# Kernel tuning notes

Hardware: AMD Instinct MI355X
Metric: run time of the kernel (lower is better)

## Reference

```python
import jax, jax.numpy as jnp
import numpy as np

N_NODES = 100000
N_EDGES = 1600000
D_IN = 64
D_OUT = 64


def setup_inputs() -> dict:
    key = jax.random.key(0)
    k1, k2, k3 = jax.random.split(key, 3)
    edge_index = jax.random.randint(k1, (2, N_EDGES), 0, N_NODES, dtype=jnp.int64)
    x = jax.random.normal(k2, (N_NODES, D_IN), dtype=jnp.float32)
    W = jax.random.normal(k3, (D_OUT, D_IN), dtype=jnp.float32) * (1.0 / np.sqrt(D_IN))
    return {"edge_index": edge_index, "x": x, "W": W}


def reference(edge_index, x, W):
    # GCN forward: h = W x, then out = D^{-1/2} A D^{-1/2} h (symmetric normalization
    # of the COO edge list, matching normalize_edge_index + CSR SpMM in the original).
    N = x.shape[0]
    row, col = edge_index[0], edge_index[1]
    # degree from row occurrences of the adjacency
    deg = jax.ops.segment_sum(jnp.ones(row.shape, x.dtype), row, num_segments=N)
    dinv_sqrt = jnp.where(deg > 0, 1.0 / jnp.sqrt(deg), 0.0)
    w = dinv_sqrt[row] * dinv_sqrt[col]  # [E] edge weights
    xh = x @ W.T                          # dense linear, bias=False  [N, D_OUT]
    # SpMM: out[r] = sum_e w_e * xh[col_e] for edges with row_e == r
    out = jax.ops.segment_sum(w[:, None] * xh[col], row, num_segments=N)
    return out
```

## Files before the change

kernel.cpp:

```cpp
#include <hip/hip_runtime.h>
#include <hip/hip_fp16.h>

#define D     64
#define RPB   256
#define BCAP  4608
#define EPB   2048
#define NBMAX 400

typedef __attribute__((ext_vector_type(8))) _Float16 f16x8;
typedef __attribute__((ext_vector_type(4))) float    f32x4;

__global__ __launch_bounds__(256) void bucket_kernel(const int* __restrict__ ei, int E,
                                                     int nb,
                                                     int* __restrict__ cursor,
                                                     int* __restrict__ bbuf) {
    __shared__ int hist[NBMAX];
    __shared__ int base_l[NBMAX];
    __shared__ int stage_v[EPB];
    __shared__ unsigned short stage_b[EPB];
    int tid = threadIdx.x;

    for (int i = tid; i < nb; i += 256) hist[i] = 0;
    __syncthreads();

    long long e0 = (long long)blockIdx.x * EPB;
#pragma unroll
    for (int i = 0; i < EPB / 256; ++i) {
        int idx = i * 256 + tid;
        long long e = e0 + idx;
        unsigned short b = 0xFFFF;
        int v = 0;
        if (e < E) {
            int r = ei[e];
            int c = ei[E + e];
            b = (unsigned short)(r >> 8);
            v = ((r & (RPB - 1)) << 17) | c;
            atomicAdd(&hist[b], 1);
        }
        stage_v[idx] = v;
        stage_b[idx] = b;
    }
    __syncthreads();

    for (int i = tid; i < nb; i += 256) {
        int c = hist[i];
        base_l[i] = (c > 0) ? atomicAdd(&cursor[i], c) : 0;
        hist[i] = 0;
    }
    __syncthreads();

#pragma unroll
    for (int i = 0; i < EPB / 256; ++i) {
        int idx = i * 256 + tid;
        unsigned short b = stage_b[idx];
        if (b != 0xFFFF) {
            int off = base_l[b] + atomicAdd(&hist[b], 1);
            if (off < BCAP)
                bbuf[(size_t)b * BCAP + off] = stage_v[idx];
        }
    }
}

__global__ __launch_bounds__(512) void sort_kernel(const int* __restrict__ cursor,
                                                   int* __restrict__ bbuf,
                                                   float* __restrict__ dinv,
                                                   int2* __restrict__ rowinfo, int N) {
    __shared__ int sorted[BCAP];
    __shared__ int hist[RPB];
    __shared__ int pfx[RPB];
    __shared__ int curs[RPB];
    int b = blockIdx.x, tid = threadIdx.x;
    int cnt = min(cursor[b], BCAP);
    int* gbuf = bbuf + (size_t)b * BCAP;

    if (tid < RPB) hist[tid] = 0;
    __syncthreads();
    for (int j = tid; j < cnt; j += 512) atomicAdd(&hist[gbuf[j] >> 17], 1);
    __syncthreads();

    int dv = 0;
    if (tid < RPB) { dv = hist[tid]; pfx[tid] = dv; }
    __syncthreads();
    for (int off = 1; off < RPB; off <<= 1) {
        int add = 0;
        if (tid < RPB && tid >= off) add = pfx[tid - off];
        __syncthreads();
        if (tid < RPB) pfx[tid] += add;
        __syncthreads();
    }

    if (tid < RPB) {
        int excl = pfx[tid] - dv;
        int r = (b << 8) + tid;
        if (r < N) {
            dinv[r] = (dv > 0) ? rsqrtf((float)dv) : 0.0f;
            rowinfo[r] = make_int2(b * BCAP + excl, dv);
        }
        curs[tid] = excl;
    }
    __syncthreads();

    for (int j = tid; j < cnt; j += 512) {
        int v = gbuf[j];
        int pos = atomicAdd(&curs[v >> 17], 1);
        sorted[pos] = v;
    }
    __syncthreads();
    for (int j = tid; j < cnt; j += 512) gbuf[j] = sorted[j];
}

__global__ __launch_bounds__(256) void linear_kernel(const float* __restrict__ x,
                                                     const float* __restrict__ W,
                                                     const float* __restrict__ dinv,
                                                     __half* __restrict__ xh, int M) {
    int tid  = threadIdx.x;
    int lane = tid & 63;
    int wv   = tid >> 6;
    int r16  = lane & 15;
    int quad = lane >> 4;

    if (blockIdx.x == 0 && tid < D) xh[(size_t)M * D + tid] = __float2half(0.0f);

    f16x8 Bf[4][2];
#pragma unroll
    for (int g = 0; g < 4; ++g)
#pragma unroll
        for (int s = 0; s < 2; ++s) {
            const float4* wp = (const float4*)(W + (size_t)(16 * g + r16) * D + 32 * s + quad * 8);
            float4 w0 = wp[0], w1 = wp[1];
            f16x8 h;
            h[0] = (_Float16)w0.x; h[1] = (_Float16)w0.y;
            h[2] = (_Float16)w0.z; h[3] = (_Float16)w0.w;
            h[4] = (_Float16)w1.x; h[5] = (_Float16)w1.y;
            h[6] = (_Float16)w1.z; h[7] = (_Float16)w1.w;
            Bf[g][s] = h;
        }

    int ntiles = (M + 15) / 16;
    int stride = gridDim.x * 4;
    for (int t = blockIdx.x * 4 + wv; t < ntiles; t += stride) {
        int r0 = t * 16;
        int ra = min(r0 + r16, M - 1);
        const float4* xp = (const float4*)(x + (size_t)ra * D + quad * 8);
        float4 a0 = xp[0], a1 = xp[1], a2 = xp[8], a3 = xp[9];
        f16x8 A0, A1;
        A0[0] = (_Float16)a0.x; A0[1] = (_Float16)a0.y; A0[2] = (_Float16)a0.z; A0[3] = (_Float16)a0.w;
        A0[4] = (_Float16)a1.x; A0[5] = (_Float16)a1.y; A0[6] = (_Float16)a1.z; A0[7] = (_Float16)a1.w;
        A1[0] = (_Float16)a2.x; A1[1] = (_Float16)a2.y; A1[2] = (_Float16)a2.z; A1[3] = (_Float16)a2.w;
        A1[4] = (_Float16)a3.x; A1[5] = (_Float16)a3.y; A1[6] = (_Float16)a3.z; A1[7] = (_Float16)a3.w;

        f32x4 acc[4];
#pragma unroll
        for (int g = 0; g < 4; ++g) {
            f32x4 z = {0.f, 0.f, 0.f, 0.f};
            z = __builtin_amdgcn_mfma_f32_16x16x32_f16(A0, Bf[g][0], z, 0, 0, 0);
            acc[g] = __builtin_amdgcn_mfma_f32_16x16x32_f16(A1, Bf[g][1], z, 0, 0, 0);
        }

#pragma unroll
        for (int reg = 0; reg < 4; ++reg) {
            int rr = r0 + quad * 4 + reg;
            if (rr < M) {
                float dvr = dinv[rr];
                __half* op = xh + (size_t)rr * D + r16;
#pragma unroll
                for (int g = 0; g < 4; ++g)
                    op[16 * g] = __float2half(dvr * acc[g][reg]);
            }
        }
    }
}

__global__ __launch_bounds__(256) void spmm_kernel(const int2* __restrict__ rowinfo,
                                                   const int* __restrict__ bbuf,
                                                   const float* __restrict__ dinv,
                                                   const __half2* __restrict__ xh2,
                                                   float2* __restrict__ out2, int N) {
    int r = (blockIdx.x * 256 + threadIdx.x) >> 6;
    if (r >= N) return;
    int c   = threadIdx.x & 63;
    int sub = c >> 5;
    int f   = c & 31;

    int2 ri   = rowinfo[r];
    int start = ri.x;
    int d     = ri.y;
    float dr  = dinv[r];

    float ax = 0.f, ay = 0.f;
    for (int j0 = 0; j0 < d; j0 += 64) {
        int n = d - j0;
        if (n > 64) n = 64;
        int cn_reg = (c < n) ? (bbuf[start + j0 + c] & 0x1FFFF) : N;
        int n16 = (n + 15) & ~15;
        for (int k = 0; k < n16; k += 16) {
            int e0 = __shfl(cn_reg, k +  0 + sub);
            int e1 = __shfl(cn_reg, k +  2 + sub);
            int e2 = __shfl(cn_reg, k +  4 + sub);
            int e3 = __shfl(cn_reg, k +  6 + sub);
            int e4 = __shfl(cn_reg, k +  8 + sub);
            int e5 = __shfl(cn_reg, k + 10 + sub);
            int e6 = __shfl(cn_reg, k + 12 + sub);
            int e7 = __shfl(cn_reg, k + 14 + sub);
            float2 v0 = __half22float2(xh2[(size_t)e0 * 32 + f]);
            float2 v1 = __half22float2(xh2[(size_t)e1 * 32 + f]);
            float2 v2 = __half22float2(xh2[(size_t)e2 * 32 + f]);
            float2 v3 = __half22float2(xh2[(size_t)e3 * 32 + f]);
            float2 v4 = __half22float2(xh2[(size_t)e4 * 32 + f]);
            float2 v5 = __half22float2(xh2[(size_t)e5 * 32 + f]);
            float2 v6 = __half22float2(xh2[(size_t)e6 * 32 + f]);
            float2 v7 = __half22float2(xh2[(size_t)e7 * 32 + f]);
            ax += ((v0.x + v1.x) + (v2.x + v3.x)) + ((v4.x + v5.x) + (v6.x + v7.x));
            ay += ((v0.y + v1.y) + (v2.y + v3.y)) + ((v4.y + v5.y) + (v6.y + v7.y));
        }
    }
    float sx = ax + __shfl(ax, c ^ 32);
    float sy = ay + __shfl(ay, c ^ 32);
    if (sub == 0) {
        float2 res = make_float2(dr * sx, dr * sy);
        __builtin_nontemporal_store(__builtin_bit_cast(double, res),
                                    (double*)&out2[(size_t)r * 32 + f]);
    }
}

extern "C" void kernel_launch(void* const* d_in, const int* in_sizes, int n_in,
                              void* d_out, int out_size, void* d_ws, size_t ws_size,
                              hipStream_t stream) {
    const int*   ei = (const int*)d_in[0];
    const float* x  = (const float*)d_in[1];
    const float* W  = (const float*)d_in[2];
    float* out = (float*)d_out;

    int E  = in_sizes[0] / 2;
    int N  = in_sizes[1] / D;
    int nb = (N + RPB - 1) / RPB;

    char* p = (char*)d_ws;
    size_t off = 0;
    auto take = [&](size_t bytes) -> char* {
        char* cur = p + off;
        off = (off + bytes + 255) & ~(size_t)255;
        return cur;
    };
    float*  dinv    = (float*)take((size_t)N * 4);
    int2*   rowinfo = (int2*)take((size_t)N * 8);
    int*    cursor  = (int*)take((size_t)nb * 4);
    int*    bbuf    = (int*)take((size_t)nb * BCAP * 4);
    __half* xh      = (__half*)take((size_t)(N + 1) * D * 2);
    (void)ws_size;

    hipMemsetAsync(cursor, 0, (size_t)nb * 4, stream);

    bucket_kernel<<<(E + EPB - 1) / EPB, 256, 0, stream>>>(ei, E, nb, cursor, bbuf);
    sort_kernel<<<nb, 512, 0, stream>>>(cursor, bbuf, dinv, rowinfo, N);
    linear_kernel<<<1024, 256, 0, stream>>>(x, W, dinv, xh, N);
    spmm_kernel<<<(N + 3) / 4, 256, 0, stream>>>(rowinfo, bbuf, dinv,
                                                 (const __half2*)xh, (float2*)out, N);
}
```

Baseline: 166.0 us.

## Persistent SpMM with prefetched row info, shuffle scan in sort, leaner bucketing

The SpMM kernel becomes a grid-stride persistent kernel. Each wave prefetches row info two rows ahead and the first 64 column indices one row ahead, so the latency of those dependent loads overlaps with gathering the current row. Row info widens to int4 to carry the inverse sqrt degree, which removes a separate dinv load. The sort kernel swaps its barrier-heavy LDS prefix scan for a wave shuffle scan, and the bucket kernel drops LDS staging, re-reading the edge list in its second pass with larger blocks of 512 threads over 4096 edges.

Measured after the change: 164.7 us. About the same (-0.8%).

```diff
diff --git a/kernel.cpp b/kernel.cpp
--- a/kernel.cpp
+++ b/kernel.cpp
@@ -4,71 +4,55 @@
 #define D     64
 #define RPB   256
 #define BCAP  4608
-#define EPB   2048
+#define EPB   4096
 #define NBMAX 400
 
 typedef __attribute__((ext_vector_type(8))) _Float16 f16x8;
 typedef __attribute__((ext_vector_type(4))) float    f32x4;
 
-__global__ __launch_bounds__(256) void bucket_kernel(const int* __restrict__ ei, int E,
+__global__ __launch_bounds__(512) void bucket_kernel(const int* __restrict__ ei, int E,
                                                      int nb,
                                                      int* __restrict__ cursor,
                                                      int* __restrict__ bbuf) {
     __shared__ int hist[NBMAX];
     __shared__ int base_l[NBMAX];
-    __shared__ int stage_v[EPB];
-    __shared__ unsigned short stage_b[EPB];
     int tid = threadIdx.x;
 
-    for (int i = tid; i < nb; i += 256) hist[i] = 0;
-    __syncthreads();
-
-    long long e0 = (long long)blockIdx.x * EPB;
-#pragma unroll
-    for (int i = 0; i < EPB / 256; ++i) {
-        int idx = i * 256 + tid;
-        long long e = e0 + idx;
-        unsigned short b = 0xFFFF;
-        int v = 0;
-        if (e < E) {
-            int r = ei[e];
-            int c = ei[E + e];
-            b = (unsigned short)(r >> 8);
-            v = ((r & (RPB - 1)) << 17) | c;
-            atomicAdd(&hist[b], 1);
-        }
-        stage_v[idx] = v;
-        stage_b[idx] = b;
-    }
-    __syncthreads();
-
-    for (int i = tid; i < nb; i += 256) {
+    for (int i = tid; i < nb; i += 512) hist[i] = 0;
+    __syncthreads();
+
+    int e0 = blockIdx.x * EPB;
+    int n  = min(EPB, E - e0);
+
+    for (int idx = tid; idx < n; idx += 512)
+        atomicAdd(&hist[ei[e0 + idx] >> 8], 1);
+    __syncthreads();
+
+    for (int i = tid; i < nb; i += 512) {
         int c = hist[i];
         base_l[i] = (c > 0) ? atomicAdd(&cursor[i], c) : 0;
         hist[i] = 0;
     }
     __syncthreads();
 
-#pragma unroll
-    for (int i = 0; i < EPB / 256; ++i) {
-        int idx = i * 256 + tid;
-        unsigned short b = stage_b[idx];
-        if (b != 0xFFFF) {
-            int off = base_l[b] + atomicAdd(&hist[b], 1);
-            if (off < BCAP)
-                bbuf[(size_t)b * BCAP + off] = stage_v[idx];
-        }
+    for (int idx = tid; idx < n; idx += 512) {
+        int r = ei[e0 + idx];
+        int c = ei[E + e0 + idx];
+        int b = r >> 8;
+        int off = base_l[b] + atomicAdd(&hist[b], 1);
+        if (off < BCAP)
+            bbuf[(size_t)b * BCAP + off] = ((r & (RPB - 1)) << 17) | c;
     }
 }
 
 __global__ __launch_bounds__(512) void sort_kernel(const int* __restrict__ cursor,
                                                    int* __restrict__ bbuf,
                                                    float* __restrict__ dinv,
-                                                   int2* __restrict__ rowinfo, int N) {
+                                                   int4* __restrict__ rowinfo, int N) {
     __shared__ int sorted[BCAP];
     __shared__ int hist[RPB];
-    __shared__ int pfx[RPB];
     __shared__ int curs[RPB];
+    __shared__ int wsum[4];
     int b = blockIdx.x, tid = threadIdx.x;
     int cnt = min(cursor[b], BCAP);
     int* gbuf = bbuf + (size_t)b * BCAP;
@@ -78,23 +62,29 @@
     for (int j = tid; j < cnt; j += 512) atomicAdd(&hist[gbuf[j] >> 17], 1);
     __syncthreads();
 
-    int dv = 0;
-    if (tid < RPB) { dv = hist[tid]; pfx[tid] = dv; }
-    __syncthreads();
-    for (int off = 1; off < RPB; off <<= 1) {
-        int add = 0;
-        if (tid < RPB && tid >= off) add = pfx[tid - off];
-        __syncthreads();
-        if (tid < RPB) pfx[tid] += add;
-        __syncthreads();
-    }
-
+    int dv = 0, s = 0;
     if (tid < RPB) {
-        int excl = pfx[tid] - dv;
+        dv = hist[tid];
+        s = dv;
+#pragma unroll
+        for (int off = 1; off < 64; off <<= 1) {
+            int t = __shfl_up(s, off);
+            if ((tid & 63) >= off) s += t;
+        }
+        if ((tid & 63) == 63) wsum[tid >> 6] = s;
+    }
+    __syncthreads();
+    if (tid < RPB) {
+        int woff = 0;
+#pragma unroll
+        for (int i = 0; i < 3; ++i)
+            if ((tid >> 6) > i) woff += wsum[i];
+        int excl = s + woff - dv;
         int r = (b << 8) + tid;
         if (r < N) {
-            dinv[r] = (dv > 0) ? rsqrtf((float)dv) : 0.0f;
-            rowinfo[r] = make_int2(b * BCAP + excl, dv);
+            float di = (dv > 0) ? rsqrtf((float)dv) : 0.0f;
+            dinv[r] = di;
+            rowinfo[r] = make_int4(b * BCAP + excl, dv, __float_as_int(di), 0);
         }
         curs[tid] = excl;
     }
@@ -171,37 +161,44 @@
     }
 }
 
-__global__ __launch_bounds__(256) void spmm_kernel(const int2* __restrict__ rowinfo,
+__global__ __launch_bounds__(256) void spmm_kernel(const int4* __restrict__ rowinfo,
                                                    const int* __restrict__ bbuf,
-                                                   const float* __restrict__ dinv,
                                                    const __half2* __restrict__ xh2,
-                                                   float2* __restrict__ out2, int N) {
-    int r = (blockIdx.x * 256 + threadIdx.x) >> 6;
-    if (r >= N) return;
+                                                   float2* __restrict__ out2,
+                                                   int N, int stride) {
+    int wid = (blockIdx.x * 256 + threadIdx.x) >> 6;
     int c   = threadIdx.x & 63;
     int sub = c >> 5;
     int f   = c & 31;
 
-    int2 ri   = rowinfo[r];
-    int start = ri.x;
-    int d     = ri.y;
-    float dr  = dinv[r];
-
-    float ax = 0.f, ay = 0.f;
-    for (int j0 = 0; j0 < d; j0 += 64) {
-        int n = d - j0;
-        if (n > 64) n = 64;
-        int cn_reg = (c < n) ? (bbuf[start + j0 + c] & 0x1FFFF) : N;
+    int r0 = wid;
+    if (r0 >= N) return;
+
+    int4 ri0 = rowinfo[r0];
+    int4 ri1 = (r0 + stride < N) ? rowinfo[r0 + stride] : make_int4(0, 0, 0, 0);
+    int  cn0 = (c < min(ri0.y, 64)) ? (bbuf[ri0.x + c] & 0x1FFFF) : N;
+
+    for (int r = r0; r < N; r += stride) {
+        int rn  = r + stride;
+        int rn2 = rn + stride;
+        int4 ri2 = (rn2 < N) ? rowinfo[rn2] : make_int4(0, 0, 0, 0);
+        int  cn1 = (rn < N && c < min(ri1.y, 64)) ? (bbuf[ri1.x + c] & 0x1FFFF) : N;
+
+        int   d  = ri0.y;
+        float dr = __int_as_float(ri0.z);
+        float ax = 0.f, ay = 0.f;
+
+        int n = min(d, 64);
         int n16 = (n + 15) & ~15;
         for (int k = 0; k < n16; k += 16) {
-            int e0 = __shfl(cn_reg, k +  0 + sub);
-            int e1 = __shfl(cn_reg, k +  2 + sub);
-            int e2 = __shfl(cn_reg, k +  4 + sub);
-            int e3 = __shfl(cn_reg, k +  6 + sub);
-            int e4 = __shfl(cn_reg, k +  8 + sub);
-            int e5 = __shfl(cn_reg, k + 10 + sub);
-            int e6 = __shfl(cn_reg, k + 12 + sub);
-            int e7 = __shfl(cn_reg, k + 14 + sub);
+            int e0 = __shfl(cn0, k +  0 + sub);
+            int e1 = __shfl(cn0, k +  2 + sub);
+            int e2 = __shfl(cn0, k +  4 + sub);
+            int e3 = __shfl(cn0, k +  6 + sub);
+            int e4 = __shfl(cn0, k +  8 + sub);
+            int e5 = __shfl(cn0, k + 10 + sub);
+            int e6 = __shfl(cn0, k + 12 + sub);
+            int e7 = __shfl(cn0, k + 14 + sub);
             float2 v0 = __half22float2(xh2[(size_t)e0 * 32 + f]);
             float2 v1 = __half22float2(xh2[(size_t)e1 * 32 + f]);
             float2 v2 = __half22float2(xh2[(size_t)e2 * 32 + f]);
@@ -213,13 +210,40 @@
             ax += ((v0.x + v1.x) + (v2.x + v3.x)) + ((v4.x + v5.x) + (v6.x + v7.x));
             ay += ((v0.y + v1.y) + (v2.y + v3.y)) + ((v4.y + v5.y) + (v6.y + v7.y));
         }
-    }
-    float sx = ax + __shfl(ax, c ^ 32);
-    float sy = ay + __shfl(ay, c ^ 32);
-    if (sub == 0) {
-        float2 res = make_float2(dr * sx, dr * sy);
-        __builtin_nontemporal_store(__builtin_bit_cast(double, res),
-                                    (double*)&out2[(size_t)r * 32 + f]);
+        for (int j0 = 64; j0 < d; j0 += 64) {
+            int nn = min(d - j0, 64);
+            int cnx = (c < nn) ? (bbuf[ri0.x + j0 + c] & 0x1FFFF) : N;
+            int m16 = (nn + 15) & ~15;
+            for (int k = 0; k < m16; k += 16) {
+                int e0 = __shfl(cnx, k +  0 + sub);
+                int e1 = __shfl(cnx, k +  2 + sub);
+                int e2 = __shfl(cnx, k +  4 + sub);
+                int e3 = __shfl(cnx, k +  6 + sub);
+                int e4 = __shfl(cnx, k +  8 + sub);
+                int e5 = __shfl(cnx, k + 10 + sub);
+                int e6 = __shfl(cnx, k + 12 + sub);
+                int e7 = __shfl(cnx, k + 14 + sub);
+                float2 v0 = __half22float2(xh2[(size_t)e0 * 32 + f]);
+                float2 v1 = __half22float2(xh2[(size_t)e1 * 32 + f]);
+                float2 v2 = __half22float2(xh2[(size_t)e2 * 32 + f]);
+                float2 v3 = __half22float2(xh2[(size_t)e3 * 32 + f]);
+                float2 v4 = __half22float2(xh2[(size_t)e4 * 32 + f]);
+                float2 v5 = __half22float2(xh2[(size_t)e5 * 32 + f]);
+                float2 v6 = __half22float2(xh2[(size_t)e6 * 32 + f]);
+                float2 v7 = __half22float2(xh2[(size_t)e7 * 32 + f]);
+                ax += ((v0.x + v1.x) + (v2.x + v3.x)) + ((v4.x + v5.x) + (v6.x + v7.x));
+                ay += ((v0.y + v1.y) + (v2.y + v3.y)) + ((v4.y + v5.y) + (v6.y + v7.y));
+            }
+        }
+
+        float sx = ax + __shfl(ax, c ^ 32);
+        float sy = ay + __shfl(ay, c ^ 32);
+        if (sub == 0) {
+            float2 res = make_float2(dr * sx, dr * sy);
+            __builtin_nontemporal_store(__builtin_bit_cast(double, res),
+                                        (double*)&out2[(size_t)r * 32 + f]);
+        }
+        ri0 = ri1; ri1 = ri2; cn0 = cn1;
     }
 }
 
@@ -243,7 +267,7 @@
         return cur;
     };
     float*  dinv    = (float*)take((size_t)N * 4);
-    int2*   rowinfo = (int2*)take((size_t)N * 8);
+    int4*   rowinfo = (int4*)take((size_t)N * 16);
     int*    cursor  = (int*)take((size_t)nb * 4);
     int*    bbuf    = (int*)take((size_t)nb * BCAP * 4);
     __half* xh      = (__half*)take((size_t)(N + 1) * D * 2);
@@ -251,9 +275,11 @@
 
     hipMemsetAsync(cursor, 0, (size_t)nb * 4, stream);
 
-    bucket_kernel<<<(E + EPB - 1) / EPB, 256, 0, stream>>>(ei, E, nb, cursor, bbuf);
+    bucket_kernel<<<(E + EPB - 1) / EPB, 512, 0, stream>>>(ei, E, nb, cursor, bbuf);
     sort_kernel<<<nb, 512, 0, stream>>>(cursor, bbuf, dinv, rowinfo, N);
     linear_kernel<<<1024, 256, 0, stream>>>(x, W, dinv, xh, N);
-    spmm_kernel<<<(N + 3) / 4, 256, 0, stream>>>(rowinfo, bbuf, dinv,
-                                                 (const __half2*)xh, (float2*)out, N);
-}
+
+    int spmm_blocks = 3072;
+    spmm_kernel<<<spmm_blocks, 256, 0, stream>>>(rowinfo, bbuf, (const __half2*)xh,
+                                                 (float2*)out, N, spmm_blocks * 4);
+}
```
